# Performance work log

Hardware: AMD Instinct MI355X
Metric: run time of the kernel (lower is better)

The kernel has to match this reference:

```python
import jax, jax.numpy as jnp
import numpy as np

B, T = 8, 2048
DV, DA = 1024, 128          # visual / audio feature dims
D1, D2 = 512, 128           # conv1d channels
DH = D2 + DA + 1            # 257: lorentz dim after time-coord pad
DG = 128                    # per-branch GCN output dim (args.dim)
NEG = 0.01                  # LeakyReLU slope
K_CURV = 1.0
EPS = 1e-6


def leaky(x):
    return jnp.where(x >= 0, x, NEG * x)


def expmap0_lorentz(x):
    # x: [B,T,DH] with x[...,0] == 0 (tangent at origin), k = 1
    xs = x[..., 1:]
    n = jnp.sqrt(jnp.maximum(jnp.sum(xs * xs, -1, keepdims=True), 1e-12))
    return jnp.concatenate([jnp.cosh(n), jnp.sinh(n) / n * xs], axis=-1)


def lorentz_similarity(x):
    # xy_inner = -<x,x>_L  (negate time component of left factor, negate product)
    signs = jnp.concatenate([-jnp.ones((1,), x.dtype), jnp.ones((DH - 1,), x.dtype)])
    xy = -jnp.einsum('bid,bjd->bij', x * signs, x)          # [B,T,T]
    xy = jnp.maximum(xy, 1.0)                                # F.threshold(., 1, 1)
    d = (K_CURV ** 0.5) * jnp.log(xy + jnp.sqrt(xy * xy - 1.0 + 1e-7))
    return jnp.clip(d, EPS, 200.0)


def adj_fn(proj_x, seq_len):
    x2 = jnp.exp(-lorentz_similarity(proj_x))               # [B,T,T]
    pos = jnp.arange(T)
    row = pos[None, :, None] < seq_len[:, None, None]       # [B,T,1]
    col = pos[None, None, :] < seq_len[:, None, None]       # [B,1,T]
    thr = jnp.where(x2 > 0.8, x2, 0.0)                      # F.threshold(., 0.8, 0)
    logits = jnp.where(col, thr, -1e30)                     # softmax over valid cols
    p = jax.nn.softmax(logits, axis=-1)
    return p * (row & col)                                  # zero outside [:L,:L]


def clas_fn(logits, seq_len):
    # logits: [B,T]; per-sample top-k (k = L//16 + 1) mean, then sigmoid
    pos = jnp.arange(T)
    valid = pos[None, :] < seq_len[:, None]
    masked = jnp.where(valid, logits, -1e30)
    srt = -jnp.sort(-masked, axis=1)                         # descending
    k = seq_len // 16 + 1                                    # [B]
    kmask = pos[None, :] < k[:, None]
    mil = jnp.sum(srt * kmask, axis=1) / k.astype(logits.dtype)
    return jax.nn.sigmoid(mil)


def forward(inputs, seq_len, w1, b1, w2, b2, gw1, gw2, cls_w, cls_b):
    xv = inputs[:, :, :DV]
    xa = inputs[:, :, DV:]
    xv = leaky(jnp.einsum('btc,oc->bto', xv, w1) + b1)       # conv1d k=1
    xv = leaky(jnp.einsum('btc,oc->bto', xv, w2) + b2)
    x = jnp.concatenate([xv, xa], axis=-1)                   # [B,T,256]

    # DistanceAdj: exp(-|i-j| / e), shared across batch
    pos = jnp.arange(T, dtype=jnp.float32)
    disadj = jnp.exp(-jnp.abs(pos[:, None] - pos[None, :]) / jnp.exp(1.0))  # [T,T]

    # expm: pad time coord, lorentz expmap0
    proj_x = expmap0_lorentz(
        jnp.concatenate([jnp.zeros(x.shape[:-1] + (1,), x.dtype), x], axis=-1))  # [B,T,257]

    adj = adj_fn(proj_x, seq_len)                            # [B,T,T]

    x1 = leaky(jnp.einsum('bij,bjd->bid', adj, proj_x) @ gw1)        # HFSGCN stand-in
    x2 = leaky(jnp.einsum('ij,bjd->bid', disadj, proj_x) @ gw2)      # HTRGCN stand-in
    out_x = jnp.concatenate([x1, x2], axis=-1)               # [B,T,256]

    # HypClassifier: 2 + 2*<x, cls>_L + bias  (lorentz inner)
    signs = jnp.concatenate([-jnp.ones((1,), out_x.dtype), jnp.ones((2 * DG - 1,), out_x.dtype)])
    frame_prob = 2.0 + 2.0 * jnp.einsum('btd,cd->btc', out_x * signs, cls_w) + cls_b  # [B,T,1]

    mil_logits = clas_fn(frame_prob[..., 0], seq_len)        # [B]
    return mil_logits, frame_prob


def setup_inputs() -> dict:
    key = jax.random.key(0)
    ks = jax.random.split(key, 8)
    inputs = jax.random.normal(ks[0], (B, T, DV + DA), jnp.float32)
    seq_len = jax.random.randint(ks[1], (B,), T // 2, T + 1, jnp.int32)
    w1 = jax.random.normal(ks[2], (D1, DV), jnp.float32) / np.float32(np.sqrt(DV))
    b1 = jnp.zeros((D1,), jnp.float32)
    w2 = jax.random.normal(ks[3], (D2, D1), jnp.float32) / np.float32(np.sqrt(D1))
    b2 = jnp.zeros((D2,), jnp.float32)
    gw1 = jax.random.normal(ks[4], (DH, DG), jnp.float32) / np.float32(np.sqrt(DH))
    gw2 = jax.random.normal(ks[5], (DH, DG), jnp.float32) / np.float32(np.sqrt(DH))
    cls_w = jax.random.normal(ks[6], (1, 2 * DG), jnp.float32) / np.float32(np.sqrt(2 * DG))
    cls_b = jnp.zeros((1,), jnp.float32)
    return dict(inputs=inputs, seq_len=seq_len, w1=w1, b1=b1, w2=w2, b2=b2,
                gw1=gw1, gw2=gw2, cls_w=cls_w, cls_b=cls_b)


def reference(inputs, seq_len, w1, b1, w2, b2, gw1, gw2, cls_w, cls_b):
    return forward(inputs, seq_len, w1, b1, w2, b2, gw1, gw2, cls_w, cls_b)
```

## Files before the change

kernel.cpp:

```cpp
#include <hip/hip_runtime.h>
#include <math.h>

#define BB 8
#define TT 2048
#define DV_ 1024
#define DA_ 128
#define D1_ 512
#define D2_ 128
#define DH_ 257
#define DHP 288
#define DG_ 128
#define MTOT (BB*TT)
#define NPX ((size_t)MTOT*DHP)

#define NEGS 0.01f
#define INV_E 0.36787944117144233f
#define CH 64
#define HALO 64
#define UB 8

#define RS 40
#define BKC 32

static const size_t o_big = 0;
static const size_t o_c1  = 16777216;
static const size_t o_c2  = o_c1 + 8388608;
static const size_t o_w   = o_c2 + 2097152;
static const size_t o_S   = o_w + 663552;
static const size_t o_den = o_S + 2304;

static const size_t sw_w1h = 0;
static const size_t sw_w1l = 524288;
static const size_t sw_w2h = 1048576;
static const size_t sw_w2l = 1114112;
static const size_t sw_g1h = 1179648;
static const size_t sw_g1l = 1216512;
static const size_t sw_g2h = 1253376;
static const size_t sw_g2l = 1290240;

typedef __attribute__((ext_vector_type(8))) __bf16 bf16x8;
typedef __attribute__((ext_vector_type(8))) unsigned short us8;
typedef __attribute__((ext_vector_type(4))) float f32x4;

__device__ __forceinline__ float diag_w() {
    float dd = logf(1.0f + sqrtf(1.0f*1.0f - 1.0f + 1e-7f));
    dd = fminf(fmaxf(dd, 1e-6f), 200.0f);
    float x2 = expf(-dd);
    return expf(x2) - 1.0f;
}

__device__ __forceinline__ unsigned short f2bf(float f) {
    unsigned int u = __float_as_uint(f);
    u += 0x7FFFu + ((u >> 16) & 1u);
    return (unsigned short)(u >> 16);
}
__device__ __forceinline__ float bf2f(unsigned short h) {
    return __uint_as_float((unsigned int)h << 16);
}

__device__ __forceinline__ void cvt8(const float4 a, const float4 b,
                                     us8& h, us8& l) {
    unsigned short hh;
#define CV_(idx, val) hh = f2bf(val); h[idx] = hh; l[idx] = f2bf((val) - bf2f(hh));
    CV_(0, a.x) CV_(1, a.y) CV_(2, a.z) CV_(3, a.w)
    CV_(4, b.x) CV_(5, b.y) CV_(6, b.z) CV_(7, b.w)
#undef CV_
}

__global__ void k_init(float* __restrict__ den, const int* __restrict__ seq,
                       float* __restrict__ S) {
    int r = blockIdx.x * 256 + threadIdx.x;
    den[r] = (float)seq[r >> 11] + diag_w();
    if (r < BB * DHP) S[r] = 0.f;
}

__global__ void k_split_w(const float* __restrict__ w1, const float* __restrict__ w2,
                          unsigned short* __restrict__ h1, unsigned short* __restrict__ l1,
                          unsigned short* __restrict__ h2, unsigned short* __restrict__ l2) {
    size_t i = ((size_t)blockIdx.x * 256 + threadIdx.x) * 4;
    const float* src; unsigned short *h, *l; size_t o;
    if (i < (size_t)D1_ * DV_) { src = w1; h = h1; l = l1; o = i; }
    else {
        o = i - (size_t)D1_ * DV_;
        if (o >= (size_t)D2_ * D1_) return;
        src = w2; h = h2; l = l2;
    }
    float4 v = *(const float4*)(src + o);
    ushort4 hv, lv;
    hv.x = f2bf(v.x); lv.x = f2bf(v.x - bf2f(hv.x));
    hv.y = f2bf(v.y); lv.y = f2bf(v.y - bf2f(hv.y));
    hv.z = f2bf(v.z); lv.z = f2bf(v.z - bf2f(hv.z));
    hv.w = f2bf(v.w); lv.w = f2bf(v.w - bf2f(hv.w));
    *(ushort4*)(h + o) = hv;
    *(ushort4*)(l + o) = lv;
}

__global__ void k_padgw_t(const float* __restrict__ g1, const float* __restrict__ g2,
                          unsigned short* __restrict__ h1, unsigned short* __restrict__ l1,
                          unsigned short* __restrict__ h2, unsigned short* __restrict__ l2) {
    int i = blockIdx.x * 256 + threadIdx.x;
    if (i >= DG_ * DHP) return;
    const float* g = blockIdx.y ? g2 : g1;
    unsigned short* th = blockIdx.y ? h2 : h1;
    unsigned short* tl = blockIdx.y ? l2 : l1;
    int c = i / DHP, k = i - c * DHP;
    float v = (k < DH_) ? g[k * DG_ + c] : 0.f;
    unsigned short hh = f2bf(v);
    th[i] = hh;
    tl[i] = f2bf(v - bf2f(hh));
}

__global__ __launch_bounds__(256, 4) void gemm_mlp1(
    const float* __restrict__ inA,
    const unsigned short* __restrict__ Bh, const unsigned short* __restrict__ Bl,
    const float* __restrict__ bias,
    unsigned short* __restrict__ Ch, unsigned short* __restrict__ Cl)
{
    __shared__ unsigned short sm[2][2][64 * RS];
    const int ib = blockIdx.x;
    const int x = ib & 7, slot = ib >> 3;
    const int cc = slot & 3, g = slot >> 2;
    const int row0 = (x + 8 * g) * 64, col0 = cc * 128;
    const int tid = threadIdx.x;
    const int wave = tid >> 6, lane = tid & 63;
    const int c0 = col0 + wave * 32;
    const int q = lane >> 4, m = lane & 15;
    const int srow = tid >> 2, scol = (tid & 3) << 3;
    const size_t gA0 = (size_t)(row0 + srow) * 1152 + scol;
    const int s0 = srow * RS + scol;
    size_t bo_[2];
#pragma unroll
    for (int t = 0; t < 2; ++t) bo_[t] = (size_t)(c0 + t*16 + m) * DV_ + q*8;

    float4 a00, a01;
    bf16x8 fah[4], fal[4];
    bf16x8 bh0[2], bl0[2], bh1[2], bl1[2];

#define M1_LDGA(o) { \
    a00 = *(const float4*)(inA + gA0 + (o)); a01 = *(const float4*)(inA + gA0 + (o) + 4); }
#define M1_STAGE(BUF) { \
    us8 h_, l_; \
    cvt8(a00, a01, h_, l_); \
    *(us8*)&sm[BUF][0][s0] = h_; *(us8*)&sm[BUF][1][s0] = l_; }
#define M1_LDGB(S, o) \
    _Pragma("unroll") \
    for (int t = 0; t < 2; ++t) { \
        bh##S[t] = *(const bf16x8*)(Bh + bo_[t] + (o)); \
        bl##S[t] = *(const bf16x8*)(Bl + bo_[t] + (o)); }
#define M1_LOADA(BUF) \
    _Pragma("unroll") \
    for (int t = 0; t < 4; ++t) { \
        const int ra = (t*16 + m) * RS + q*8; \
        fah[t] = *(const bf16x8*)&sm[BUF][0][ra]; \
        fal[t] = *(const bf16x8*)&sm[BUF][1][ra]; }
#define M1_MFMA(S) \
    _Pragma("unroll") \
    for (int mi = 0; mi < 4; ++mi) \
        _Pragma("unroll") \
        for (int nj = 0; nj < 2; ++nj) { \
            acc[mi][nj] = __builtin_amdgcn_mfma_f32_16x16x32_bf16(fah[mi], bh##S[nj], acc[mi][nj], 0, 0, 0); \
            acc[mi][nj] = __builtin_amdgcn_mfma_f32_16x16x32_bf16(fal[mi], bh##S[nj], acc[mi][nj], 0, 0, 0); \
            acc[mi][nj] = __builtin_amdgcn_mfma_f32_16x16x32_bf16(fah[mi], bl##S[nj], acc[mi][nj], 0, 0, 0); \
        }

    f32x4 acc[4][2];
#pragma unroll
    for (int a = 0; a < 4; ++a)
#pragma unroll
        for (int c = 0; c < 2; ++c) acc[a][c] = (f32x4){0.f, 0.f, 0.f, 0.f};

    M1_LDGA(0)
    M1_STAGE(0)
    M1_LDGB(0, 0)
    __syncthreads();

    const int NI = (DV_ / BKC) / 2;
    for (int i = 0; i < NI; ++i) {
        const size_t o1 = (size_t)(2*i + 1) * BKC;
        M1_LDGA(o1)
        M1_LDGB(1, o1)
        M1_LOADA(0)
        M1_MFMA(0)
        M1_STAGE(1)
        __syncthreads();
        if (i + 1 < NI) {
            const size_t o2 = (size_t)(2*i + 2) * BKC;
            M1_LDGA(o2)
            M1_LDGB(0, o2)
        }
        M1_LOADA(1)
        M1_MFMA(1)
        if (i + 1 < NI) { M1_STAGE(0) }
        __syncthreads();
    }
#undef M1_LDGA
#undef M1_STAGE
#undef M1_LDGB
#undef M1_LOADA
#undef M1_MFMA

    float bj[2];
#pragma unroll
    for (int nj = 0; nj < 2; ++nj) bj[nj] = bias[c0 + nj*16 + m];
#pragma unroll
    for (int mi = 0; mi < 4; ++mi)
#pragma unroll
        for (int nj = 0; nj < 2; ++nj)
#pragma unroll
            for (int t = 0; t < 4; ++t) {
                int i = row0 + mi*16 + q*4 + t;
                int j = c0 + nj*16 + m;
                float v = acc[mi][nj][t] + bj[nj];
                v = (v >= 0.f) ? v : NEGS * v;
                size_t o = (size_t)i * D1_ + j;
                unsigned short hh = f2bf(v);
                Ch[o] = hh;
                Cl[o] = f2bf(v - bf2f(hh));
            }
}

#define LOADK2(S, k0, LD) \
    _Pragma("unroll") \
    for (int t = 0; t < 4; ++t) { \
        size_t ao = (size_t)(r0 + t*16 + m) * (LD) + (k0) + q*8; \
        ah##S[t] = *(const bf16x8*)(Ah + ao); \
        al##S[t] = *(const bf16x8*)(Al + ao); \
    } \
    _Pragma("unroll") \
    for (int t = 0; t < 2; ++t) { \
        size_t bo = (size_t)(c0 + t*16 + m) * (LD) + (k0) + q*8; \
        bh##S[t] = *(const bf16x8*)(Bh + bo); \
        bl##S[t] = *(const bf16x8*)(Bl + bo); \
    }
#define MFMAK2(S) \
    _Pragma("unroll") \
    for (int mi = 0; mi < 4; ++mi) \
        _Pragma("unroll") \
        for (int nj = 0; nj < 2; ++nj) { \
            acc[mi][nj] = __builtin_amdgcn_mfma_f32_16x16x32_bf16(ah##S[mi], bh##S[nj], acc[mi][nj], 0, 0, 0); \
            acc[mi][nj] = __builtin_amdgcn_mfma_f32_16x16x32_bf16(al##S[mi], bh##S[nj], acc[mi][nj], 0, 0, 0); \
            acc[mi][nj] = __builtin_amdgcn_mfma_f32_16x16x32_bf16(ah##S[mi], bl##S[nj], acc[mi][nj], 0, 0, 0); \
        }

__global__ __launch_bounds__(256, 1) void gemm_mlp2(
    const unsigned short* __restrict__ Ah, const unsigned short* __restrict__ Al,
    const unsigned short* __restrict__ Bh, const unsigned short* __restrict__ Bl,
    const float* __restrict__ bias, float* __restrict__ Cf)
{
    const int row0 = blockIdx.x * 64;
    const int wave = threadIdx.x >> 6, lane = threadIdx.x & 63;
    const int r0 = row0, c0 = wave * 32;
    const int q = lane >> 4, m = lane & 15;
    f32x4 acc[4][2];
#pragma unroll
    for (int a = 0; a < 4; ++a)
#pragma unroll
        for (int c = 0; c < 2; ++c) acc[a][c] = (f32x4){0.f, 0.f, 0.f, 0.f};
    bf16x8 ah0[4], al0[4], bh0[2], bl0[2];
    bf16x8 ah1[4], al1[4], bh1[2], bl1[2];
    LOADK2(0, 0, D1_)
    for (int k0 = 0; k0 + 64 <= D1_; k0 += 64) {
        LOADK2(1, k0 + 32, D1_)
        MFMAK2(0)
        if (k0 + 64 < D1_) { LOADK2(0, k0 + 64, D1_) }
        MFMAK2(1)
    }
    float bj[2];
#pragma unroll
    for (int nj = 0; nj < 2; ++nj) bj[nj] = bias[c0 + nj*16 + m];
#pragma unroll
    for (int mi = 0; mi < 4; ++mi)
#pragma unroll
        for (int nj = 0; nj < 2; ++nj)
#pragma unroll
            for (int t = 0; t < 4; ++t) {
                int i = r0 + mi*16 + q*4 + t;
                int j = c0 + nj*16 + m;
                float v = acc[mi][nj][t] + bj[nj];
                v = (v >= 0.f) ? v : NEGS * v;
                Cf[(size_t)i * D2_ + j] = v;
            }
}

__global__ __launch_bounds__(256, 1) void gemm_gc(
    const unsigned short* __restrict__ A1h, const unsigned short* __restrict__ A1l,
    const unsigned short* __restrict__ A2h, const unsigned short* __restrict__ A2l,
    const unsigned short* __restrict__ G1h, const unsigned short* __restrict__ G1l,
    const unsigned short* __restrict__ G2h, const unsigned short* __restrict__ G2l,
    float* __restrict__ X1, float* __restrict__ X2)
{
    const int z = blockIdx.z;
    const unsigned short* Ah = z ? A2h : A1h;
    const unsigned short* Al = z ? A2l : A1l;
    const unsigned short* Bh = z ? G2h : G1h;
    const unsigned short* Bl = z ? G2l : G1l;
    float* Cf = z ? X2 : X1;
    const int row0 = blockIdx.y * 64;
    const int wave = threadIdx.x >> 6, lane = threadIdx.x & 63;
    const int r0 = row0, c0 = wave * 32;
    const int q = lane >> 4, m = lane & 15;
    f32x4 acc[4][2];
#pragma unroll
    for (int a = 0; a < 4; ++a)
#pragma unroll
        for (int c = 0; c < 2; ++c) acc[a][c] = (f32x4){0.f, 0.f, 0.f, 0.f};
    bf16x8 ah0[4], al0[4], bh0[2], bl0[2];
    bf16x8 ah1[4], al1[4], bh1[2], bl1[2];
    LOADK2(0, 0, DHP)
    int k0 = 0;
    for (; k0 + 64 <= DHP; k0 += 64) {
        LOADK2(1, k0 + 32, DHP)
        MFMAK2(0)
        if (k0 + 64 < DHP) { LOADK2(0, k0 + 64, DHP) }
        MFMAK2(1)
    }
    if (k0 < DHP) { MFMAK2(0) }
#pragma unroll
    for (int mi = 0; mi < 4; ++mi)
#pragma unroll
        for (int nj = 0; nj < 2; ++nj)
#pragma unroll
            for (int t = 0; t < 4; ++t) {
                int i = r0 + mi*16 + q*4 + t;
                int j = c0 + nj*16 + m;
                float v = acc[mi][nj][t];
                v = (v >= 0.f) ? v : NEGS * v;
                Cf[(size_t)i * DG_ + j] = v;
            }
}

#define XLOAD(S, k0) \
    _Pragma("unroll") \
    for (int t = 0; t < 4; ++t) { \
        af##S[t] = *(const bf16x8*)(base + (size_t)(r0 + t*16 + m) * DHP + (k0) + q*8); \
        bf##S[t] = *(const bf16x8*)(base + (size_t)(c0 + t*16 + m) * DHP + (k0) + q*8); \
    }
#define XMFMA(S) \
    _Pragma("unroll") \
    for (int mi = 0; mi < 4; ++mi) \
        _Pragma("unroll") \
        for (int nj = 0; nj < 4; ++nj) \
            acc[mi][nj] = __builtin_amdgcn_mfma_f32_16x16x32_bf16(af##S[mi], bf##S[nj], acc[mi][nj], 0, 0, 0);

__global__ __launch_bounds__(256, 1) void k_xy_mfma(
    const unsigned short* __restrict__ pxb, const float* __restrict__ px,
    const int* __restrict__ seq, float* __restrict__ den, float* __restrict__ accb)
{
    const int b = blockIdx.z;
    const int bx = blockIdx.x, by = blockIdx.y;
    if (bx < by) return;
    const int nb = seq[b];
    const int row0 = by * 128, col0 = bx * 128;
    if (row0 >= nb || col0 >= nb) return;
    const int wave = threadIdx.x >> 6, lane = threadIdx.x & 63;
    const int r0 = row0 + (wave >> 1) * 64, c0 = col0 + (wave & 1) * 64;
    if (c0 + 63 < r0 || r0 >= nb || c0 >= nb) return;
    const unsigned short* base = pxb + (size_t)b * TT * DHP;
    const int q = lane >> 4, m = lane & 15;
    f32x4 acc[4][4];
#pragma unroll
    for (int a = 0; a < 4; ++a)
#pragma unroll
        for (int c = 0; c < 4; ++c) acc[a][c] = (f32x4){0.f, 0.f, 0.f, 0.f};
    bf16x8 af0[4], bf0[4], af1[4], bf1[4];
    XLOAD(0, 0)
    int k0 = 0;
    for (; k0 + 64 <= DHP; k0 += 64) {
        XLOAD(1, k0 + 32)
        XMFMA(0)
        if (k0 + 64 < DHP) { XLOAD(0, k0 + 64) }
        XMFMA(1)
    }
    if (k0 < DHP) { XMFMA(0) }
    const float* b32 = px + (size_t)b * TT * DHP;
    float cj[4], ci[4][4];
#pragma unroll
    for (int nj = 0; nj < 4; ++nj) cj[nj] = b32[(size_t)(c0 + nj*16 + m) * DHP];
#pragma unroll
    for (int mi = 0; mi < 4; ++mi)
#pragma unroll
        for (int t = 0; t < 4; ++t) ci[mi][t] = b32[(size_t)(r0 + mi*16 + q*4 + t) * DHP];
#pragma unroll
    for (int mi = 0; mi < 4; ++mi)
#pragma unroll
        for (int nj = 0; nj < 4; ++nj)
#pragma unroll
            for (int t = 0; t < 4; ++t) {
                int i = r0 + mi*16 + q*4 + t;
                int j = c0 + nj*16 + m;
                if (i < j && j < nb) {
                    float xyv = 2.f * ci[mi][t] * cj[nj] - acc[mi][nj][t];
                    float xym = fmaxf(xyv, 1.0f);
                    if (xym < 1.026f) {
                        float dd = logf(xym + sqrtf(xym * xym - 1.0f + 1e-7f));
                        dd = fminf(fmaxf(dd, 1e-6f), 200.0f);
                        float x2v = expf(-dd);
                        if (x2v > 0.8f) {
                            float w = expf(x2v) - 1.0f;
                            atomicAdd(&den[b * TT + i], w);
                            atomicAdd(&den[b * TT + j], w);
                            const float* pi = b32 + (size_t)i * DHP;
                            const float* pj = b32 + (size_t)j * DHP;
                            float* ai = accb + ((size_t)(b * TT + i)) * DHP;
                            float* aj = accb + ((size_t)(b * TT + j)) * DHP;
                            for (int d = 0; d < DHP; ++d) {
                                atomicAdd(&ai[d], w * pj[d]);
                                atomicAdd(&aj[d], w * pi[d]);
                            }
                        }
                    }
                }
            }
}

__global__ __launch_bounds__(256) void k_proj(
    const float* __restrict__ C2, const float* __restrict__ inputs,
    float* __restrict__ px, unsigned short* __restrict__ pxb,
    float* __restrict__ accb)
{
    const int r = blockIdx.x;
    const int tid = threadIdx.x;
    float v = (tid < 128) ? C2[(size_t)r * 128 + tid]
                          : inputs[(size_t)r * 1152 + 1024 + (tid - 128)];
    float sq = v * v;
#pragma unroll
    for (int o = 32; o > 0; o >>= 1) sq += __shfl_down(sq, o, 64);
    __shared__ float wred[4];
    __shared__ float cs[2];
    if ((tid & 63) == 0) wred[tid >> 6] = sq;
    __syncthreads();
    if (tid == 0) {
        float n2 = fmaxf(wred[0] + wred[1] + wred[2] + wred[3], 1e-12f);
        float n = sqrtf(n2);
        cs[0] = coshf(n);
        cs[1] = sinhf(n) / n;
    }
    __syncthreads();
    float sv = cs[1] * v;
    px[(size_t)r * DHP + 1 + tid] = sv;
    pxb[(size_t)r * DHP + 1 + tid] = f2bf(sv);
    if (tid == 0) {
        px[(size_t)r * DHP] = cs[0];
        pxb[(size_t)r * DHP] = f2bf(cs[0]);
    }
    if (tid < DHP - DH_) {
        px[(size_t)r * DHP + DH_ + tid] = 0.f;
        pxb[(size_t)r * DHP + DH_ + tid] = 0;
    }
    float* ab = accb + (size_t)r * DHP;
    ab[tid] = 0.f;
    if (tid < DHP - 256) ab[256 + tid] = 0.f;
}

__global__ __launch_bounds__(256) void k_ssum(
    const float* __restrict__ px, const int* __restrict__ seq,
    float* __restrict__ S)
{
    const int b = blockIdx.x, chunk = blockIdx.y, tid = threadIdx.x;
    const int nb = seq[b];
    const int j0 = chunk * 32;
    const int j1 = (j0 + 32 < nb) ? j0 + 32 : nb;
    float a0 = 0.f, a1 = 0.f;
    const bool hasB = (tid < DHP - 256);
    for (int j = j0; j < j1; ++j) {
        const float* row = px + ((size_t)(b * TT + j)) * DHP;
        a0 += row[tid];
        if (hasB) a1 += row[256 + tid];
    }
    if (j1 > j0) {
        atomicAdd(&S[b * DHP + tid], a0);
        if (hasB) atomicAdd(&S[b * DHP + 256 + tid], a1);
    }
}

__global__ void k_y1(const float* __restrict__ accb, const float* __restrict__ S,
                     const float* __restrict__ den, const int* __restrict__ seq,
                     const float* __restrict__ px,
                     unsigned short* __restrict__ yh, unsigned short* __restrict__ yl)
{
    size_t idx = (size_t)blockIdx.x * 256 + threadIdx.x;
    if (idx >= NPX) return;
    int r = (int)(idx / DHP);
    int b = r >> 11, i = r & (TT - 1);
    int d = (int)(idx - (size_t)r * DHP);
    float out = 0.f;
    if (i < seq[b])
        out = (S[b * DHP + d] + accb[idx] + diag_w() * px[idx]) / den[r];
    unsigned short hh = f2bf(out);
    yh[idx] = hh;
    yl[idx] = f2bf(out - bf2f(hh));
}

__global__ __launch_bounds__(256) void k_band(
    const float* __restrict__ px,
    unsigned short* __restrict__ yh, unsigned short* __restrict__ yl)
{
    __shared__ float Fs[CH][DHP];
    const int b = blockIdx.y;
    const int i0 = blockIdx.x * CH;
    const int tid = threadIdx.x;
    const bool hasB = (tid < DHP - 256);
    const float r = expf(-INV_E);
    const float* base = px + (size_t)b * TT * DHP;

    {
        const int jlo = (i0 - HALO > 0) ? i0 - HALO : 0;
        float LA = 0.f, LB = 0.f;
        for (int j = jlo; j < i0 + CH; j += UB) {
            float va[UB], vb[UB];
#pragma unroll
            for (int u = 0; u < UB; ++u) {
                const float* row = base + (size_t)(j + u) * DHP;
                va[u] = row[tid];
                vb[u] = hasB ? row[256 + tid] : 0.f;
            }
#pragma unroll
            for (int u = 0; u < UB; ++u) {
                LA = fmaf(r, LA, va[u]);
                LB = fmaf(r, LB, vb[u]);
                const int jj = j + u;
                if (jj >= i0) {
                    Fs[jj - i0][tid] = LA;
                    if (hasB) Fs[jj - i0][256 + tid] = LB;
                }
            }
        }
    }
    __syncthreads();
    {
        const int jhi = (i0 + CH - 1 + HALO < TT - 1) ? i0 + CH - 1 + HALO : TT - 1;
        float RA = 0.f, RB = 0.f;
        int j = jhi;
        for (; j >= i0 + CH; j -= UB) {
            float va[UB], vb[UB];
#pragma unroll
            for (int u = 0; u < UB; ++u) {
                const float* row = base + (size_t)(j - u) * DHP;
                va[u] = row[tid];
                vb[u] = hasB ? row[256 + tid] : 0.f;
            }
#pragma unroll
            for (int u = 0; u < UB; ++u) {
                RA = fmaf(r, RA, va[u]);
                RB = fmaf(r, RB, vb[u]);
            }
        }
        for (; j >= i0; j -= UB) {
            float va[UB], vb[UB];
#pragma unroll
            for (int u = 0; u < UB; ++u) {
                const float* row = base + (size_t)(j - u) * DHP;
                va[u] = row[tid];
                vb[u] = hasB ? row[256 + tid] : 0.f;
            }
#pragma unroll
            for (int u = 0; u < UB; ++u) {
                const int jj = j - u;
                RA = fmaf(r, RA, va[u]);
                RB = fmaf(r, RB, vb[u]);
                size_t o = ((size_t)(b * TT + jj)) * DHP + tid;
                float ya = Fs[jj - i0][tid] + RA - va[u];
                unsigned short hh = f2bf(ya);
                yh[o] = hh; yl[o] = f2bf(ya - bf2f(hh));
                if (hasB) {
                    float yb = Fs[jj - i0][256 + tid] + RB - vb[u];
                    size_t ob = o + 256;
                    unsigned short h2 = f2bf(yb);
                    yh[ob] = h2; yl[ob] = f2bf(yb - bf2f(h2));
                }
            }
        }
    }
}

__global__ __launch_bounds__(256) void k_frame(
    const float* __restrict__ x1, const float* __restrict__ x2f,
    const float* __restrict__ cls_w, const float* __restrict__ cls_b,
    float* __restrict__ dout)
{
    const int r = blockIdx.x * 4 + (threadIdx.x >> 6);
    const int lane = threadIdx.x & 63;
    float s = 0.f;
#pragma unroll
    for (int t = 0; t < 2; ++t) {
        int g = lane + t * 64;
        float cw1 = cls_w[g];
        if (g == 0) cw1 = -cw1;
        s += x1[(size_t)r * DG_ + g] * cw1;
        s += x2f[(size_t)r * DG_ + g] * cls_w[DG_ + g];
    }
#pragma unroll
    for (int o = 32; o > 0; o >>= 1) s += __shfl_down(s, o, 64);
    if (lane == 0) dout[8 + r] = 2.0f + 2.0f * s + cls_b[0];
}

__global__ __launch_bounds__(1024) void k_clas(
    const int* __restrict__ seq, float* __restrict__ dout)
{
    __shared__ float s[TT];
    const int b = blockIdx.x, tid = threadIdx.x;
    const int nb = seq[b];
    for (int t = tid; t < TT; t += 1024)
        s[t] = (t < nb) ? dout[8 + b * TT + t] : -1e30f;
    __syncthreads();
    for (int k = 2; k <= TT; k <<= 1)
        for (int j = k >> 1; j > 0; j >>= 1) {
            for (int i = tid; i < TT; i += 1024) {
                int ixj = i ^ j;
                if (ixj > i) {
                    float a = s[i], c = s[ixj];
                    bool descBlk = ((i & k) == 0);
                    if (descBlk ? (a < c) : (a > c)) { s[i] = c; s[ixj] = a; }
                }
            }
            __syncthreads();
        }
    const int kk = nb / 16 + 1;
    float part = 0.f;
    for (int t = tid; t < kk; t += 1024) part += s[t];
#pragma unroll
    for (int o = 32; o > 0; o >>= 1) part += __shfl_down(part, o, 64);
    __shared__ float wred[16];
    if ((tid & 63) == 0) wred[tid >> 6] = part;
    __syncthreads();
    if (tid == 0) {
        float mil = 0.f;
#pragma unroll
        for (int t = 0; t < 16; ++t) mil += wred[t];
        mil /= (float)kk;
        dout[b] = 1.f / (1.f + expf(-mil));
    }
}

extern "C" void kernel_launch(void* const* d_in, const int* in_sizes, int n_in,
                              void* d_out, int out_size, void* d_ws, size_t ws_size,
                              hipStream_t stream) {
    (void)in_sizes; (void)n_in; (void)out_size; (void)ws_size;
    const float* inputs = (const float*)d_in[0];
    const int*   seq    = (const int*)d_in[1];
    const float* w1     = (const float*)d_in[2];
    const float* b1     = (const float*)d_in[3];
    const float* w2     = (const float*)d_in[4];
    const float* b2     = (const float*)d_in[5];
    const float* gw1    = (const float*)d_in[6];
    const float* gw2    = (const float*)d_in[7];
    const float* cls_w  = (const float*)d_in[8];
    const float* cls_b  = (const float*)d_in[9];
    float* dout = (float*)d_out;
    float* ws = (float*)d_ws;

    float* px  = ws + o_big;
    unsigned short* pxb = (unsigned short*)(ws + o_big + 4718592);
    unsigned short* y2h = (unsigned short*)(ws + o_big + 7077888);
    unsigned short* y2l = y2h + NPX;
    unsigned short* y1h = (unsigned short*)(ws + o_big + 11796480);
    unsigned short* y1l = y1h + NPX;
    unsigned short* C1h = (unsigned short*)(ws + o_c1);
    unsigned short* C1l = C1h + (size_t)MTOT * D1_;
    float* accb = ws + o_c1;
    float* x1   = ws + o_c1 + 4718592;
    float* C2  = ws + o_c2;
    float* x2f = ws + o_c2;
    unsigned short* wsS = (unsigned short*)(ws + o_w);
    unsigned short *W1h = wsS + sw_w1h, *W1l = wsS + sw_w1l;
    unsigned short *W2h = wsS + sw_w2h, *W2l = wsS + sw_w2l;
    unsigned short *g1h = wsS + sw_g1h, *g1l = wsS + sw_g1l;
    unsigned short *g2h = wsS + sw_g2h, *g2l = wsS + sw_g2l;
    float* S   = ws + o_S;
    float* den = ws + o_den;

    k_init<<<MTOT / 256, 256, 0, stream>>>(den, seq, S);
    k_split_w<<<576, 256, 0, stream>>>(w1, w2, W1h, W1l, W2h, W2l);
    k_padgw_t<<<dim3(144, 2), 256, 0, stream>>>(gw1, gw2, g1h, g1l, g2h, g2l);

    gemm_mlp1<<<1024, 256, 0, stream>>>(inputs, W1h, W1l, b1, C1h, C1l);
    gemm_mlp2<<<256, 256, 0, stream>>>(C1h, C1l, W2h, W2l, b2, C2);

    k_proj<<<MTOT, 256, 0, stream>>>(C2, inputs, px, pxb, accb);

    k_ssum<<<dim3(BB, TT / 32), 256, 0, stream>>>(px, seq, S);

    k_xy_mfma<<<dim3(TT / 128, TT / 128, BB), 256, 0, stream>>>(pxb, px, seq, den, accb);

    k_y1<<<(int)(NPX / 256), 256, 0, stream>>>(accb, S, den, seq, px, y1h, y1l);

    k_band<<<dim3(TT / CH, BB), 256, 0, stream>>>(px, y2h, y2l);

    gemm_gc<<<dim3(1, MTOT / 64, 2), 256, 0, stream>>>(
        y1h, y1l, y2h, y2l, g1h, g1l, g2h, g2l, x1, x2f);

    k_frame<<<MTOT / 4, 256, 0, stream>>>(x1, x2f, cls_w, cls_b, dout);
    k_clas<<<BB, 1024, 0, stream>>>(seq, dout);
}
```

Measured before the change: 410.8 us.

## Merge setup kernels, fuse y1 normalization into GCN GEMM, enlarge mlp1 tiles

Merges the three small setup kernels into one launch. Folds the k_y1 normalization and bf16 split into the A-operand load of the first gemm_gc branch, so the y1 buffers are never written to or read back from global memory. Doubles gemm_mlp1's row tile to 128 with 512-thread blocks, giving each B fragment more reuse. In exchange, the fused GEMM reads fp32 inputs element-wise with a divide per element, and its row loads are uncoalesced scalar loads rather than vector loads.

```diff
diff --git a/kernel.cpp b/kernel.cpp
--- a/kernel.cpp
+++ b/kernel.cpp
@@ -67,63 +67,68 @@
 #undef CV_
 }
 
-__global__ void k_init(float* __restrict__ den, const int* __restrict__ seq,
-                       float* __restrict__ S) {
-    int r = blockIdx.x * 256 + threadIdx.x;
-    den[r] = (float)seq[r >> 11] + diag_w();
-    if (r < BB * DHP) S[r] = 0.f;
-}
-
-__global__ void k_split_w(const float* __restrict__ w1, const float* __restrict__ w2,
-                          unsigned short* __restrict__ h1, unsigned short* __restrict__ l1,
-                          unsigned short* __restrict__ h2, unsigned short* __restrict__ l2) {
-    size_t i = ((size_t)blockIdx.x * 256 + threadIdx.x) * 4;
-    const float* src; unsigned short *h, *l; size_t o;
-    if (i < (size_t)D1_ * DV_) { src = w1; h = h1; l = l1; o = i; }
-    else {
-        o = i - (size_t)D1_ * DV_;
-        if (o >= (size_t)D2_ * D1_) return;
-        src = w2; h = h2; l = l2;
-    }
-    float4 v = *(const float4*)(src + o);
-    ushort4 hv, lv;
-    hv.x = f2bf(v.x); lv.x = f2bf(v.x - bf2f(hv.x));
-    hv.y = f2bf(v.y); lv.y = f2bf(v.y - bf2f(hv.y));
-    hv.z = f2bf(v.z); lv.z = f2bf(v.z - bf2f(hv.z));
-    hv.w = f2bf(v.w); lv.w = f2bf(v.w - bf2f(hv.w));
-    *(ushort4*)(h + o) = hv;
-    *(ushort4*)(l + o) = lv;
-}
-
-__global__ void k_padgw_t(const float* __restrict__ g1, const float* __restrict__ g2,
-                          unsigned short* __restrict__ h1, unsigned short* __restrict__ l1,
-                          unsigned short* __restrict__ h2, unsigned short* __restrict__ l2) {
-    int i = blockIdx.x * 256 + threadIdx.x;
-    if (i >= DG_ * DHP) return;
-    const float* g = blockIdx.y ? g2 : g1;
-    unsigned short* th = blockIdx.y ? h2 : h1;
-    unsigned short* tl = blockIdx.y ? l2 : l1;
-    int c = i / DHP, k = i - c * DHP;
-    float v = (k < DH_) ? g[k * DG_ + c] : 0.f;
-    unsigned short hh = f2bf(v);
-    th[i] = hh;
-    tl[i] = f2bf(v - bf2f(hh));
-}
-
-__global__ __launch_bounds__(256, 4) void gemm_mlp1(
+__global__ void k_setup(float* __restrict__ den, const int* __restrict__ seq,
+                        float* __restrict__ S,
+                        const float* __restrict__ w1, const float* __restrict__ w2,
+                        unsigned short* __restrict__ h1, unsigned short* __restrict__ l1,
+                        unsigned short* __restrict__ h2, unsigned short* __restrict__ l2,
+                        const float* __restrict__ g1, const float* __restrict__ g2,
+                        unsigned short* __restrict__ gh1, unsigned short* __restrict__ gl1,
+                        unsigned short* __restrict__ gh2, unsigned short* __restrict__ gl2)
+{
+    const int bx = blockIdx.x;
+    if (bx < 64) {
+        int r = bx * 256 + threadIdx.x;
+        den[r] = (float)seq[r >> 11] + diag_w();
+        if (r < BB * DHP) S[r] = 0.f;
+    } else if (bx < 640) {
+        size_t i = ((size_t)(bx - 64) * 256 + threadIdx.x) * 4;
+        const float* src; unsigned short *h, *l; size_t o;
+        if (i < (size_t)D1_ * DV_) { src = w1; h = h1; l = l1; o = i; }
+        else {
+            o = i - (size_t)D1_ * DV_;
+            if (o >= (size_t)D2_ * D1_) return;
+            src = w2; h = h2; l = l2;
+        }
+        float4 v = *(const float4*)(src + o);
+        ushort4 hv, lv;
+        hv.x = f2bf(v.x); lv.x = f2bf(v.x - bf2f(hv.x));
+        hv.y = f2bf(v.y); lv.y = f2bf(v.y - bf2f(hv.y));
+        hv.z = f2bf(v.z); lv.z = f2bf(v.z - bf2f(hv.z));
+        hv.w = f2bf(v.w); lv.w = f2bf(v.w - bf2f(hv.w));
+        *(ushort4*)(h + o) = hv;
+        *(ushort4*)(l + o) = lv;
+    } else {
+        const int bb = bx - 640;
+        const int zz = (bb >= 144);
+        int i = (bb - (zz ? 144 : 0)) * 256 + threadIdx.x;
+        if (i >= DG_ * DHP) return;
+        const float* g = zz ? g2 : g1;
+        unsigned short* th = zz ? gh2 : gh1;
+        unsigned short* tl = zz ? gl2 : gl1;
+        int c = i / DHP, k = i - c * DHP;
+        float v = (k < DH_) ? g[k * DG_ + c] : 0.f;
+        unsigned short hh = f2bf(v);
+        th[i] = hh;
+        tl[i] = f2bf(v - bf2f(hh));
+    }
+}
+
+__global__ __launch_bounds__(512, 2) void gemm_mlp1(
     const float* __restrict__ inA,
     const unsigned short* __restrict__ Bh, const unsigned short* __restrict__ Bl,
     const float* __restrict__ bias,
     unsigned short* __restrict__ Ch, unsigned short* __restrict__ Cl)
 {
-    __shared__ unsigned short sm[2][2][64 * RS];
+    __shared__ unsigned short sm[2][2][128 * RS];
     const int ib = blockIdx.x;
     const int x = ib & 7, slot = ib >> 3;
     const int cc = slot & 3, g = slot >> 2;
-    const int row0 = (x + 8 * g) * 64, col0 = cc * 128;
+    const int row0 = (x + 8 * g) * 128, col0 = cc * 128;
     const int tid = threadIdx.x;
     const int wave = tid >> 6, lane = tid & 63;
-    const int c0 = col0 + wave * 32;
+    const int r0w = (wave >> 2) * 64;
+    const int c0 = col0 + (wave & 3) * 32;
     const int q = lane >> 4, m = lane & 15;
     const int srow = tid >> 2, scol = (tid & 3) << 3;
     const size_t gA0 = (size_t)(row0 + srow) * 1152 + scol;
@@ -150,7 +155,7 @@
 #define M1_LOADA(BUF) \
     _Pragma("unroll") \
     for (int t = 0; t < 4; ++t) { \
-        const int ra = (t*16 + m) * RS + q*8; \
+        const int ra = (r0w + t*16 + m) * RS + q*8; \
         fah[t] = *(const bf16x8*)&sm[BUF][0][ra]; \
         fal[t] = *(const bf16x8*)&sm[BUF][1][ra]; }
 #define M1_MFMA(S) \
@@ -208,7 +213,7 @@
         for (int nj = 0; nj < 2; ++nj)
 #pragma unroll
             for (int t = 0; t < 4; ++t) {
-                int i = row0 + mi*16 + q*4 + t;
+                int i = row0 + r0w + mi*16 + q*4 + t;
                 int j = c0 + nj*16 + m;
                 float v = acc[mi][nj][t] + bj[nj];
                 v = (v >= 0.f) ? v : NEGS * v;
@@ -283,18 +288,15 @@
 }
 
 __global__ __launch_bounds__(256, 1) void gemm_gc(
-    const unsigned short* __restrict__ A1h, const unsigned short* __restrict__ A1l,
+    const float* __restrict__ accb, const float* __restrict__ S,
+    const float* __restrict__ den, const int* __restrict__ seq,
+    const float* __restrict__ pxf,
     const unsigned short* __restrict__ A2h, const unsigned short* __restrict__ A2l,
     const unsigned short* __restrict__ G1h, const unsigned short* __restrict__ G1l,
     const unsigned short* __restrict__ G2h, const unsigned short* __restrict__ G2l,
     float* __restrict__ X1, float* __restrict__ X2)
 {
     const int z = blockIdx.z;
-    const unsigned short* Ah = z ? A2h : A1h;
-    const unsigned short* Al = z ? A2l : A1l;
-    const unsigned short* Bh = z ? G2h : G1h;
-    const unsigned short* Bl = z ? G2l : G1l;
-    float* Cf = z ? X2 : X1;
     const int row0 = blockIdx.y * 64;
     const int wave = threadIdx.x >> 6, lane = threadIdx.x & 63;
     const int r0 = row0, c0 = wave * 32;
@@ -306,27 +308,92 @@
         for (int c = 0; c < 2; ++c) acc[a][c] = (f32x4){0.f, 0.f, 0.f, 0.f};
     bf16x8 ah0[4], al0[4], bh0[2], bl0[2];
     bf16x8 ah1[4], al1[4], bh1[2], bl1[2];
-    LOADK2(0, 0, DHP)
-    int k0 = 0;
-    for (; k0 + 64 <= DHP; k0 += 64) {
-        LOADK2(1, k0 + 32, DHP)
-        MFMAK2(0)
-        if (k0 + 64 < DHP) { LOADK2(0, k0 + 64, DHP) }
-        MFMAK2(1)
-    }
-    if (k0 < DHP) { MFMAK2(0) }
-#pragma unroll
-    for (int mi = 0; mi < 4; ++mi)
-#pragma unroll
-        for (int nj = 0; nj < 2; ++nj)
-#pragma unroll
-            for (int t = 0; t < 4; ++t) {
-                int i = r0 + mi*16 + q*4 + t;
-                int j = c0 + nj*16 + m;
-                float v = acc[mi][nj][t];
-                v = (v >= 0.f) ? v : NEGS * v;
-                Cf[(size_t)i * DG_ + j] = v;
-            }
+
+    if (z == 0) {
+        const unsigned short* Bh = G1h;
+        const unsigned short* Bl = G1l;
+        const int b = row0 >> 11;
+        const int nb = seq[b];
+        const float* Sb = S + b * DHP;
+        float dn[4]; bool vl[4];
+#pragma unroll
+        for (int t = 0; t < 4; ++t) {
+            int rr = r0 + t*16 + m;
+            vl[t] = (rr & (TT - 1)) < nb;
+            dn[t] = den[rr];
+        }
+#define GLOADF(Sx, k0) \
+    _Pragma("unroll") \
+    for (int t = 0; t < 4; ++t) { \
+        const int rr = r0 + t*16 + m; \
+        const float* ap = accb + (size_t)rr * DHP + (k0) + q*8; \
+        const float* pp = pxf  + (size_t)rr * DHP + (k0) + q*8; \
+        const float* sp = Sb + (k0) + q*8; \
+        us8 h_, l_; \
+        _Pragma("unroll") \
+        for (int e = 0; e < 8; ++e) { \
+            float out = 0.f; \
+            if (vl[t]) out = (sp[e] + ap[e] + diag_w() * pp[e]) / dn[t]; \
+            unsigned short hh = f2bf(out); \
+            h_[e] = hh; l_[e] = f2bf(out - bf2f(hh)); \
+        } \
+        ah##Sx[t] = *(bf16x8*)&h_; al##Sx[t] = *(bf16x8*)&l_; \
+    } \
+    _Pragma("unroll") \
+    for (int t = 0; t < 2; ++t) { \
+        size_t bo = (size_t)(c0 + t*16 + m) * DHP + (k0) + q*8; \
+        bh##Sx[t] = *(const bf16x8*)(Bh + bo); \
+        bl##Sx[t] = *(const bf16x8*)(Bl + bo); \
+    }
+        GLOADF(0, 0)
+        int k0 = 0;
+        for (; k0 + 64 <= DHP; k0 += 64) {
+            GLOADF(1, k0 + 32)
+            MFMAK2(0)
+            if (k0 + 64 < DHP) { GLOADF(0, k0 + 64) }
+            MFMAK2(1)
+        }
+        if (k0 < DHP) { MFMAK2(0) }
+#undef GLOADF
+#pragma unroll
+        for (int mi = 0; mi < 4; ++mi)
+#pragma unroll
+            for (int nj = 0; nj < 2; ++nj)
+#pragma unroll
+                for (int t = 0; t < 4; ++t) {
+                    int i = r0 + mi*16 + q*4 + t;
+                    int j = c0 + nj*16 + m;
+                    float v = acc[mi][nj][t];
+                    v = (v >= 0.f) ? v : NEGS * v;
+                    X1[(size_t)i * DG_ + j] = v;
+                }
+    } else {
+        const unsigned short* Ah = A2h;
+        const unsigned short* Al = A2l;
+        const unsigned short* Bh = G2h;
+        const unsigned short* Bl = G2l;
+        LOADK2(0, 0, DHP)
+        int k0 = 0;
+        for (; k0 + 64 <= DHP; k0 += 64) {
+            LOADK2(1, k0 + 32, DHP)
+            MFMAK2(0)
+            if (k0 + 64 < DHP) { LOADK2(0, k0 + 64, DHP) }
+            MFMAK2(1)
+        }
+        if (k0 < DHP) { MFMAK2(0) }
+#pragma unroll
+        for (int mi = 0; mi < 4; ++mi)
+#pragma unroll
+            for (int nj = 0; nj < 2; ++nj)
+#pragma unroll
+                for (int t = 0; t < 4; ++t) {
+                    int i = r0 + mi*16 + q*4 + t;
+                    int j = c0 + nj*16 + m;
+                    float v = acc[mi][nj][t];
+                    v = (v >= 0.f) ? v : NEGS * v;
+                    X2[(size_t)i * DG_ + j] = v;
+                }
+    }
 }
 
 #define XLOAD(S, k0) \
@@ -473,24 +540,6 @@
     }
 }
 
-__global__ void k_y1(const float* __restrict__ accb, const float* __restrict__ S,
-                     const float* __restrict__ den, const int* __restrict__ seq,
-                     const float* __restrict__ px,
-                     unsigned short* __restrict__ yh, unsigned short* __restrict__ yl)
-{
-    size_t idx = (size_t)blockIdx.x * 256 + threadIdx.x;
-    if (idx >= NPX) return;
-    int r = (int)(idx / DHP);
-    int b = r >> 11, i = r & (TT - 1);
-    int d = (int)(idx - (size_t)r * DHP);
-    float out = 0.f;
-    if (i < seq[b])
-        out = (S[b * DHP + d] + accb[idx] + diag_w() * px[idx]) / den[r];
-    unsigned short hh = f2bf(out);
-    yh[idx] = hh;
-    yl[idx] = f2bf(out - bf2f(hh));
-}
-
 __global__ __launch_bounds__(256) void k_band(
     const float* __restrict__ px,
     unsigned short* __restrict__ yh, unsigned short* __restrict__ yl)
@@ -653,8 +702,6 @@
     unsigned short* pxb = (unsigned short*)(ws + o_big + 4718592);
     unsigned short* y2h = (unsigned short*)(ws + o_big + 7077888);
     unsigned short* y2l = y2h + NPX;
-    unsigned short* y1h = (unsigned short*)(ws + o_big + 11796480);
-    unsigned short* y1l = y1h + NPX;
     unsigned short* C1h = (unsigned short*)(ws + o_c1);
     unsigned short* C1l = C1h + (size_t)MTOT * D1_;
     float* accb = ws + o_c1;
@@ -669,11 +716,10 @@
     float* S   = ws + o_S;
     float* den = ws + o_den;
 
-    k_init<<<MTOT / 256, 256, 0, stream>>>(den, seq, S);
-    k_split_w<<<576, 256, 0, stream>>>(w1, w2, W1h, W1l, W2h, W2l);
-    k_padgw_t<<<dim3(144, 2), 256, 0, stream>>>(gw1, gw2, g1h, g1l, g2h, g2l);
-
-    gemm_mlp1<<<1024, 256, 0, stream>>>(inputs, W1h, W1l, b1, C1h, C1l);
+    k_setup<<<928, 256, 0, stream>>>(den, seq, S, w1, w2, W1h, W1l, W2h, W2l,
+                                     gw1, gw2, g1h, g1l, g2h, g2l);
+
+    gemm_mlp1<<<512, 512, 0, stream>>>(inputs, W1h, W1l, b1, C1h, C1l);
     gemm_mlp2<<<256, 256, 0, stream>>>(C1h, C1l, W2h, W2l, b2, C2);
 
     k_proj<<<MTOT, 256, 0, stream>>>(C2, inputs, px, pxb, accb);
@@ -682,12 +728,10 @@
 
     k_xy_mfma<<<dim3(TT / 128, TT / 128, BB), 256, 0, stream>>>(pxb, px, seq, den, accb);
 
-    k_y1<<<(int)(NPX / 256), 256, 0, stream>>>(accb, S, den, seq, px, y1h, y1l);
-
     k_band<<<dim3(TT / CH, BB), 256, 0, stream>>>(px, y2h, y2l);
 
     gemm_gc<<<dim3(1, MTOT / 64, 2), 256, 0, stream>>>(
-        y1h, y1l, y2h, y2l, g1h, g1l, g2h, g2l, x1, x2f);
+        accb, S, den, seq, px, y2h, y2l, g1h, g1l, g2h, g2l, x1, x2f);
 
     k_frame<<<MTOT / 4, 256, 0, stream>>>(x1, x2f, cls_w, cls_b, dout);
     k_clas<<<BB, 1024, 0, stream>>>(seq, dout);
```

New measurement: 457.9 us. 11.5% more time.
